# Kernel tuning notes

Hardware: AMD Instinct MI355X
Metric: run time of the kernel (lower is better)

The kernel has to match this reference:

```python
import jax, jax.numpy as jnp
import numpy as np

HEADS = 8
DIM_HEAD = 64


def setup_inputs() -> dict:
    key = jax.random.key(0)
    k1, k2, k3 = jax.random.split(key, 3)
    B, C, L = 8, 512, 8192
    hidden = HEADS * DIM_HEAD  # 512
    x = jax.random.normal(k1, (B, C, L), dtype=jnp.float32)
    W_qkv = jax.random.normal(k2, (3 * hidden, C), dtype=jnp.float32) * (1.0 / np.sqrt(C))
    W_out = jax.random.normal(k3, (C, hidden), dtype=jnp.float32) * (1.0 / np.sqrt(hidden))
    b_out = jnp.zeros((C,), dtype=jnp.float32)
    return {"x": x, "W_qkv": W_qkv, "W_out": W_out, "b_out": b_out}


def reference(x, W_qkv, W_out, b_out):
    b, c, l = x.shape
    h, d = HEADS, DIM_HEAD
    # pointwise conv1d == channel matmul: [3*h*d, c] x [b, c, l] -> [b, 3*h*d, l]
    qkv = jnp.einsum('oc,bcl->bol', W_qkv, x)
    q, k, v = jnp.split(qkv, 3, axis=1)
    q = q.reshape(b, h, d, l)
    k = jax.nn.softmax(k.reshape(b, h, d, l), axis=-1)
    v = v.reshape(b, h, d, l)
    # context = k @ v^T : [b,h,d,d]
    context = jnp.einsum('bhdl,bhel->bhde', k, v)
    # out = context^T @ q : [b,h,e,l]
    out = jnp.einsum('bhde,bhdl->bhel', context, q)
    out = out.reshape(b, h * d, l)
    # to_out pointwise conv with bias
    return jnp.einsum('ch,bhl->bcl', W_out, out) + b_out[None, :, None]
```

## Files before the change

### kernel.cpp

```cpp
#include <hip/hip_runtime.h>
#include <hip/hip_bf16.h>

typedef unsigned short u16;
typedef __attribute__((ext_vector_type(8))) short s16x8;
typedef __attribute__((ext_vector_type(4))) float f32x4;

__device__ __forceinline__ u16 f2bf(float f) {
  union { float f; unsigned u; } v; v.f = f;
  unsigned r = (v.u + 0x7fffu + ((v.u >> 16) & 1u)) >> 16;
  return (u16)r;
}
__device__ __forceinline__ float bf2f(u16 u) {
  union { unsigned u; float f; } v; v.u = ((unsigned)u) << 16;
  return v.f;
}
__device__ __forceinline__ void gld_lds16(const void* g, void* l) {
  __builtin_amdgcn_global_load_lds(
      (const __attribute__((address_space(1))) void*)g,
      (__attribute__((address_space(3))) void*)l, 16, 0, 0);
}
__device__ __forceinline__ s16x8 dsr128(const u16* p) {
  s16x8 r;
  asm volatile("ds_read_b128 %0, %1"
               : "=v"(r)
               : "v"((const __attribute__((address_space(3))) u16*)p));
  return r;
}

__global__ void prep_w(const float* __restrict__ Wqkv, const float* __restrict__ Woutf,
                       u16* __restrict__ Wkv2, u16* __restrict__ WqT, u16* __restrict__ Wout) {
  int i = blockIdx.x * 256 + threadIdx.x;
  {
    int o = i >> 9, c = i & 511;
    int h = o >> 7, r = o & 127;
    int src = (r < 64) ? (512 + h * 64 + r) : (1024 + h * 64 + (r - 64));
    Wkv2[i] = f2bf(Wqkv[src * 512 + c]);
  }
  if (i < 262144) {
    int c = i >> 9, o = i & 511;
    WqT[i]  = f2bf(Wqkv[o * 512 + c]);
    Wout[i] = f2bf(Woutf[i]);
  }
}

__global__ __launch_bounds__(256) void prep_x(const float* __restrict__ x, u16* __restrict__ xt) {
  __shared__ float t[32][33];
  int l0 = blockIdx.x * 32, c0 = blockIdx.y * 32;
  size_t b = blockIdx.z;
  int tid = threadIdx.x;
  int r = tid >> 3, q = tid & 7;
  const float4 v = *(const float4*)(x + (b * 512 + c0 + r) * 8192 + l0 + q * 4);
  t[r][q * 4 + 0] = v.x; t[r][q * 4 + 1] = v.y;
  t[r][q * 4 + 2] = v.z; t[r][q * 4 + 3] = v.w;
  __syncthreads();
  ushort4 o;
  o.x = f2bf(t[q * 4 + 0][r]); o.y = f2bf(t[q * 4 + 1][r]);
  o.z = f2bf(t[q * 4 + 2][r]); o.w = f2bf(t[q * 4 + 3][r]);
  *(ushort4*)(xt + (b * 8192 + l0 + r) * 512 + c0 + q * 4) = o;
}

__global__ __launch_bounds__(256) void gemm_bt(
    const u16* __restrict__ A, size_t sA,
    const u16* __restrict__ BT, size_t sB,
    u16* __restrict__ Cv, size_t sC,
    int N, int K)
{
  __shared__ u16 lsa[128 * 32];
  __shared__ u16 lsb[128 * 32];
  int tid = threadIdx.x, wid = tid >> 6, lane = tid & 63;
  int m0 = blockIdx.y << 7, n0 = blockIdx.x << 7;
  const u16* Ab = A + (size_t)blockIdx.z * sA;
  const u16* Bb = BT + (size_t)blockIdx.z * sB;
  int fr = lane & 15, kg = lane >> 4;
  int wr = wid >> 1, wc = wid & 1;
  int f0 = tid, f1 = tid + 256;
  const u16* pA0 = Ab + (size_t)(m0 + (f0 >> 2)) * K + (f0 & 3) * 8;
  const u16* pA1 = Ab + (size_t)(m0 + (f1 >> 2)) * K + (f1 & 3) * 8;
  const u16* pB0 = Bb + (size_t)(n0 + (f0 >> 2)) * K + (f0 & 3) * 8;
  const u16* pB1 = Bb + (size_t)(n0 + (f1 >> 2)) * K + (f1 & 3) * 8;
  u16* dA0 = &lsa[wid * 512];
  u16* dA1 = &lsa[(wid + 4) * 512];
  u16* dB0 = &lsb[wid * 512];
  u16* dB1 = &lsb[(wid + 4) * 512];
  f32x4 acc[4][4] = {};
  for (int kt = 0; kt < K; kt += 32) {
    gld_lds16(pA0, dA0); gld_lds16(pA1, dA1);
    gld_lds16(pB0, dB0); gld_lds16(pB1, dB1);
    pA0 += 32; pA1 += 32; pB0 += 32; pB1 += 32;
    __syncthreads();
    s16x8 af[4], bf_[4];
#pragma unroll
    for (int mi = 0; mi < 4; ++mi)
      af[mi] = *(const s16x8*)&lsa[(wr * 64 + mi * 16 + fr) * 32 + kg * 8];
#pragma unroll
    for (int ni = 0; ni < 4; ++ni)
      bf_[ni] = *(const s16x8*)&lsb[(wc * 64 + ni * 16 + fr) * 32 + kg * 8];
#pragma unroll
    for (int mi = 0; mi < 4; ++mi)
#pragma unroll
      for (int ni = 0; ni < 4; ++ni)
        acc[mi][ni] = __builtin_amdgcn_mfma_f32_16x16x32_bf16(af[mi], bf_[ni], acc[mi][ni], 0, 0, 0);
    __syncthreads();
  }
  int r0 = m0 + wr * 64 + kg * 4;
  int c0 = n0 + wc * 64 + fr;
  u16* C = Cv + (size_t)blockIdx.z * sC;
#pragma unroll
  for (int mi = 0; mi < 4; ++mi)
#pragma unroll
    for (int ni = 0; ni < 4; ++ni)
#pragma unroll
      for (int j = 0; j < 4; ++j)
        C[(size_t)(r0 + mi * 16 + j) * N + (c0 + ni * 16)] = f2bf(acc[mi][ni][j]);
}

__global__ __launch_bounds__(256, 4) void gemm_ctx(
    const u16* __restrict__ A,
    const u16* __restrict__ BT, size_t sB,
    float* __restrict__ E, float* __restrict__ Z)
{
  __shared__ u16 pool[17408];
  const int tid = threadIdx.x, wid = tid >> 6, lane = tid & 63;
  const int fr = lane & 15, kg = lane >> 4;
  const int wr = wid >> 1, wc = wid & 1;

  const int nwg = (int)gridDim.x;
  const int bx = (int)blockIdx.x;
  const int id = (bx & 7) * (nwg >> 3) + (bx >> 3);
  const int my = id % 8;
  const int t2 = id / 8;
  const int nx = t2 % 64;
  const int z  = t2 / 64;
  const int m0 = my << 7, n0 = nx << 7;
  const u16* Ab = A + (size_t)m0 * 512;
  const u16* Bb = BT + (size_t)z * sB + (size_t)n0 * 512;

  const int P0 = tid, P1 = tid + 256;
  int b2_, s_, t_;
  b2_ = P0 >> 3; s_ = P0 & 7; t_ = (s_ - b2_) & 7;
  const size_t g0 = (size_t)((b2_ << 1) + (t_ >> 2)) * 512 + (t_ & 3) * 8;
  b2_ = P1 >> 3; s_ = P1 & 7; t_ = (s_ - b2_) & 7;
  const size_t g1 = (size_t)((b2_ << 1) + (t_ >> 2)) * 512 + (t_ & 3) * 8;

  int aoff[4], boff[4];
#pragma unroll
  for (int i = 0; i < 4; ++i) {
    int ra = wr * 64 + i * 16 + fr;
    aoff[i] = (ra >> 1) * 64 + ((((ra & 1) << 2) + kg + (ra >> 1)) & 7) * 8;
    int rb = wc * 64 + i * 16 + fr;
    boff[i] = (rb >> 1) * 64 + ((((rb & 1) << 2) + kg + (rb >> 1)) & 7) * 8;
  }

  auto stage = [&](int sl, int kt) {
    gld_lds16(Ab + g0 + kt, &pool[sl * 4096 + P0 * 8]);
    gld_lds16(Ab + g1 + kt, &pool[sl * 4096 + P1 * 8]);
    gld_lds16(Bb + g0 + kt, &pool[8192 + sl * 4096 + P0 * 8]);
    gld_lds16(Bb + g1 + kt, &pool[8192 + sl * 4096 + P1 * 8]);
  };

  f32x4 acc[4][4] = {};
  stage(0, 0);
#pragma unroll
  for (int k = 0; k < 16; ++k) {
    if (k < 15) stage((k + 1) & 1, (k + 1) * 32);
    if (k < 15) { asm volatile("s_waitcnt vmcnt(4)" ::: "memory"); }
    else        { asm volatile("s_waitcnt vmcnt(0)" ::: "memory"); }
    __builtin_amdgcn_s_barrier();
    s16x8 af[4], bf_[4];
    const u16* la = &pool[(k & 1) * 4096];
    const u16* lb = &pool[8192 + (k & 1) * 4096];
#pragma unroll
    for (int mi = 0; mi < 4; ++mi) af[mi] = dsr128(la + aoff[mi]);
#pragma unroll
    for (int ni = 0; ni < 4; ++ni) bf_[ni] = dsr128(lb + boff[ni]);
    asm volatile("s_waitcnt lgkmcnt(0)" ::: "memory");
    __builtin_amdgcn_sched_barrier(0);
    __builtin_amdgcn_s_setprio(1);
#pragma unroll
    for (int mi = 0; mi < 4; ++mi)
#pragma unroll
      for (int ni = 0; ni < 4; ++ni)
        acc[mi][ni] = __builtin_amdgcn_mfma_f32_16x16x32_bf16(af[mi], bf_[ni], acc[mi][ni], 0, 0, 0);
    __builtin_amdgcn_s_setprio(0);
    __builtin_amdgcn_s_barrier();
  }

  const size_t bh = (size_t)z * 8 + my;
  u16* kbuf = pool;
  u16* vbuf = pool + 64 * 136;
#pragma unroll
  for (int mi = 0; mi < 4; ++mi)
#pragma unroll
    for (int ni = 0; ni < 4; ++ni)
#pragma unroll
      for (int j = 0; j < 4; ++j) {
        int r = mi * 16 + kg * 4 + j;
        int l = wc * 64 + ni * 16 + fr;
        float vv = acc[mi][ni][j];
        if (wr == 0) kbuf[r * 136 + l] = f2bf(__expf(vv));
        else         vbuf[r * 136 + l] = f2bf(vv);
      }
  __syncthreads();
  {
    int d = tid >> 2, q = tid & 3;
    float s = 0.f;
#pragma unroll
    for (int i = 0; i < 4; ++i) {
      s16x8 k8 = *(const s16x8*)&kbuf[d * 136 + q * 32 + i * 8];
#pragma unroll
      for (int j = 0; j < 8; ++j) s += bf2f((u16)k8[j]);
    }
    s += __shfl_xor(s, 1);
    s += __shfl_xor(s, 2);
    if (q == 0) atomicAdd(&Z[bh * 64 + d], s);
  }
  f32x4 eacc[4] = {};
#pragma unroll
  for (int ks = 0; ks < 4; ++ks) {
    s16x8 ka = *(const s16x8*)&kbuf[(wid * 16 + fr) * 136 + ks * 32 + kg * 8];
#pragma unroll
    for (int n2 = 0; n2 < 4; ++n2) {
      s16x8 vb = *(const s16x8*)&vbuf[(n2 * 16 + fr) * 136 + ks * 32 + kg * 8];
      eacc[n2] = __builtin_amdgcn_mfma_f32_16x16x32_bf16(ka, vb, eacc[n2], 0, 0, 0);
    }
  }
  float* Eb = E + bh * 4096;
#pragma unroll
  for (int n2 = 0; n2 < 4; ++n2)
#pragma unroll
    for (int j = 0; j < 4; ++j)
      atomicAdd(&Eb[(wid * 16 + kg * 4 + j) * 64 + n2 * 16 + fr], eacc[n2][j]);
}

__global__ __launch_bounds__(256, 4) void gemm128f(
    const u16* __restrict__ A, size_t sA,
    const u16* __restrict__ BT, size_t sB,
    float* __restrict__ Cv, size_t sC,
    const float* __restrict__ bias,
    int Mt, int Nt)
{
  __shared__ u16 lsa[2][4096];
  __shared__ u16 lsb[2][4096];
  const int tid = threadIdx.x, wid = tid >> 6, lane = tid & 63;
  const int fr = lane & 15, kg = lane >> 4;
  const int wr = wid >> 1, wc = wid & 1;

  const int nwg = (int)gridDim.x;
  const int bx = (int)blockIdx.x;
  const int id = (bx & 7) * (nwg >> 3) + (bx >> 3);
  const int my = id % Mt;
  const int t2 = id / Mt;
  const int nx = t2 % Nt;
  const int z  = t2 / Nt;
  const int m0 = my << 7, n0 = nx << 7;
  const u16* Ab = A + (size_t)z * sA;
  const u16* Bb = BT + (size_t)z * sB;

  const int P0 = tid, P1 = tid + 256;
  int b2_, s_, t_;
  b2_ = P0 >> 3; s_ = P0 & 7; t_ = (s_ - b2_) & 7;
  const size_t g0 = (size_t)((b2_ << 1) + (t_ >> 2)) * 512 + (t_ & 3) * 8;
  b2_ = P1 >> 3; s_ = P1 & 7; t_ = (s_ - b2_) & 7;
  const size_t g1 = (size_t)((b2_ << 1) + (t_ >> 2)) * 512 + (t_ & 3) * 8;
  const u16* paG0 = Ab + (size_t)m0 * 512 + g0;
  const u16* paG1 = Ab + (size_t)m0 * 512 + g1;
  const u16* pbG0 = Bb + (size_t)n0 * 512 + g0;
  const u16* pbG1 = Bb + (size_t)n0 * 512 + g1;

  int aoff[4], boff[4];
#pragma unroll
  for (int i = 0; i < 4; ++i) {
    int ra = wr * 64 + i * 16 + fr;
    aoff[i] = (ra >> 1) * 64 + ((((ra & 1) << 2) + kg + (ra >> 1)) & 7) * 8;
    int rb = wc * 64 + i * 16 + fr;
    boff[i] = (rb >> 1) * 64 + ((((rb & 1) << 2) + kg + (rb >> 1)) & 7) * 8;
  }

  auto stage = [&](int sl, int kt) {
    gld_lds16(paG0 + kt, &lsa[sl][P0 * 8]);
    gld_lds16(paG1 + kt, &lsa[sl][P1 * 8]);
    gld_lds16(pbG0 + kt, &lsb[sl][P0 * 8]);
    gld_lds16(pbG1 + kt, &lsb[sl][P1 * 8]);
  };

  f32x4 acc[4][4] = {};
  stage(0, 0);
#pragma unroll
  for (int k = 0; k < 16; ++k) {
    if (k < 15) stage((k + 1) & 1, (k + 1) * 32);
    if (k < 15) { asm volatile("s_waitcnt vmcnt(4)" ::: "memory"); }
    else        { asm volatile("s_waitcnt vmcnt(0)" ::: "memory"); }
    __builtin_amdgcn_s_barrier();
    s16x8 af[4], bf_[4];
    const u16* la = lsa[k & 1];
    const u16* lb = lsb[k & 1];
#pragma unroll
    for (int mi = 0; mi < 4; ++mi) af[mi] = dsr128(la + aoff[mi]);
#pragma unroll
    for (int ni = 0; ni < 4; ++ni) bf_[ni] = dsr128(lb + boff[ni]);
    asm volatile("s_waitcnt lgkmcnt(0)" ::: "memory");
    __builtin_amdgcn_sched_barrier(0);
    __builtin_amdgcn_s_setprio(1);
#pragma unroll
    for (int mi = 0; mi < 4; ++mi)
#pragma unroll
      for (int ni = 0; ni < 4; ++ni)
        acc[mi][ni] = __builtin_amdgcn_mfma_f32_16x16x32_bf16(af[mi], bf_[ni], acc[mi][ni], 0, 0, 0);
    __builtin_amdgcn_s_setprio(0);
    __builtin_amdgcn_s_barrier();
  }

  const int r0 = m0 + wr * 64 + kg * 4;
  const int c0 = n0 + wc * 64 + fr;
  float* C = Cv + (size_t)z * sC;
#pragma unroll
  for (int mi = 0; mi < 4; ++mi)
#pragma unroll
    for (int j = 0; j < 4; ++j) {
      float bv = bias[r0 + mi * 16 + j];
#pragma unroll
      for (int ni = 0; ni < 4; ++ni)
        C[(size_t)(r0 + mi * 16 + j) * 8192 + (c0 + ni * 16)] = acc[mi][ni][j] + bv;
    }
}

__global__ __launch_bounds__(256) void m1_fused(const float* __restrict__ E, const float* __restrict__ Z,
                                                const u16* __restrict__ Wout, u16* __restrict__ M1) {
  int cb = blockIdx.x, h = blockIdx.y, b = blockIdx.z;
  __shared__ float ctx[64][65];
  __shared__ float zs[64];
  int tid = threadIdx.x;
  size_t bh = (size_t)(b * 8 + h);
  const float* Eb = E + bh * 4096;
  if (tid < 64) zs[tid] = Z[bh * 64 + tid];
  __syncthreads();
  for (int i = tid; i < 4096; i += 256)
    ctx[i >> 6][i & 63] = Eb[i] / zs[i >> 6];
  __syncthreads();
  int d = tid & 63;
  int hbase = h * 64;
  for (int ci = 0; ci < 16; ++ci) {
    int c = __builtin_amdgcn_readfirstlane(cb * 64 + (tid >> 6) + ci * 4);
    const u16* wrow = Wout + c * 512 + hbase;
    float a0 = 0.f, a1 = 0.f, a2 = 0.f, a3 = 0.f;
#pragma unroll
    for (int e = 0; e < 64; e += 4) {
      a0 += bf2f(wrow[e + 0]) * ctx[d][e + 0];
      a1 += bf2f(wrow[e + 1]) * ctx[d][e + 1];
      a2 += bf2f(wrow[e + 2]) * ctx[d][e + 2];
      a3 += bf2f(wrow[e + 3]) * ctx[d][e + 3];
    }
    M1[((size_t)b * 512 + c) * 512 + hbase + d] = f2bf((a0 + a1) + (a2 + a3));
  }
}

extern "C" void kernel_launch(void* const* d_in, const int* in_sizes, int n_in,
                              void* d_out, int out_size, void* d_ws, size_t ws_size,
                              hipStream_t stream) {
  const float* x     = (const float*)d_in[0];
  const float* Wqkv  = (const float*)d_in[1];
  const float* Woutf = (const float*)d_in[2];
  const float* bout  = (const float*)d_in[3];
  char* ws = (char*)d_ws;
  u16*  xt  = (u16*)ws;
  u16*  Wkv2= (u16*)(ws + 201326592);
  u16*  WqT = (u16*)(ws + 202375168);
  u16*  Wo  = (u16*)(ws + 202899456);
  u16*  M1  = (u16*)(ws + 203423744);
  u16*  G   = (u16*)(ws + 207618048);
  float* E  = (float*)(ws + 211812352);
  float* Z  = (float*)(ws + 212860928);

  hipMemsetAsync(ws + 211812352, 0, 1048576 + 16384, stream);
  prep_w<<<2048, 256, 0, stream>>>(Wqkv, Woutf, Wkv2, WqT, Wo);
  prep_x<<<dim3(256, 16, 8), 256, 0, stream>>>(x, xt);
  gemm_ctx<<<4096, 256, 0, stream>>>(Wkv2, xt, (size_t)8192 * 512, E, Z);
  m1_fused<<<dim3(8, 8, 8), 256, 0, stream>>>(E, Z, Wo, M1);
  gemm_bt<<<dim3(4, 4, 8), 256, 0, stream>>>(M1, (size_t)512 * 512, WqT, 0,
                                             G, (size_t)512 * 512, 512, 512);
  gemm128f<<<2048, 256, 0, stream>>>(G, (size_t)512 * 512, xt, (size_t)8192 * 512,
                                     (float*)d_out, (size_t)512 * 8192, bout, 4, 64);
}
```

Before: 231.3 us.

## Enlarge gemm_ctx tile to 256 rows with 512-thread blocks sharing x loads

The context GEMM block now covers two heads (256 rows of K/V weights) with 8 waves instead of 128 rows with 4 waves. Each x tile loaded into LDS is reused across twice as many output rows, which halves redundant global reads of the large activation tensor and halves the grid size. In exchange the block needs twice the LDS and more threads per block, which may lower occupancy. The epilogue is extended to do the softmax sums and k·vᵀ context for two heads per block.

```diff
diff --git a/kernel.cpp b/kernel.cpp
--- a/kernel.cpp
+++ b/kernel.cpp
@@ -114,48 +114,46 @@
         C[(size_t)(r0 + mi * 16 + j) * N + (c0 + ni * 16)] = f2bf(acc[mi][ni][j]);
 }
 
-__global__ __launch_bounds__(256, 4) void gemm_ctx(
+__global__ __launch_bounds__(512, 4) void gemm_ctx(
     const u16* __restrict__ A,
     const u16* __restrict__ BT, size_t sB,
     float* __restrict__ E, float* __restrict__ Z)
 {
-  __shared__ u16 pool[17408];
+  __shared__ u16 pool[34816];
   const int tid = threadIdx.x, wid = tid >> 6, lane = tid & 63;
   const int fr = lane & 15, kg = lane >> 4;
-  const int wr = wid >> 1, wc = wid & 1;
+  const int wm = wid >> 1, wc = wid & 1;
 
   const int nwg = (int)gridDim.x;
   const int bx = (int)blockIdx.x;
   const int id = (bx & 7) * (nwg >> 3) + (bx >> 3);
-  const int my = id % 8;
-  const int t2 = id / 8;
+  const int my = id % 4;
+  const int t2 = id / 4;
   const int nx = t2 % 64;
   const int z  = t2 / 64;
-  const int m0 = my << 7, n0 = nx << 7;
+  const int m0 = my << 8, n0 = nx << 7;
   const u16* Ab = A + (size_t)m0 * 512;
   const u16* Bb = BT + (size_t)z * sB + (size_t)n0 * 512;
 
-  const int P0 = tid, P1 = tid + 256;
-  int b2_, s_, t_;
-  b2_ = P0 >> 3; s_ = P0 & 7; t_ = (s_ - b2_) & 7;
-  const size_t g0 = (size_t)((b2_ << 1) + (t_ >> 2)) * 512 + (t_ & 3) * 8;
-  b2_ = P1 >> 3; s_ = P1 & 7; t_ = (s_ - b2_) & 7;
-  const size_t g1 = (size_t)((b2_ << 1) + (t_ >> 2)) * 512 + (t_ & 3) * 8;
+  auto gsw = [](int P) -> size_t {
+    int b2 = P >> 3, s = P & 7, t = (s - b2) & 7;
+    return (size_t)((b2 << 1) + (t >> 2)) * 512 + (t & 3) * 8;
+  };
+  const size_t gA0 = gsw(tid), gA1 = gsw(tid + 512), gB0 = gsw(tid);
 
   int aoff[4], boff[4];
 #pragma unroll
   for (int i = 0; i < 4; ++i) {
-    int ra = wr * 64 + i * 16 + fr;
+    int ra = wm * 64 + i * 16 + fr;
     aoff[i] = (ra >> 1) * 64 + ((((ra & 1) << 2) + kg + (ra >> 1)) & 7) * 8;
     int rb = wc * 64 + i * 16 + fr;
     boff[i] = (rb >> 1) * 64 + ((((rb & 1) << 2) + kg + (rb >> 1)) & 7) * 8;
   }
 
   auto stage = [&](int sl, int kt) {
-    gld_lds16(Ab + g0 + kt, &pool[sl * 4096 + P0 * 8]);
-    gld_lds16(Ab + g1 + kt, &pool[sl * 4096 + P1 * 8]);
-    gld_lds16(Bb + g0 + kt, &pool[8192 + sl * 4096 + P0 * 8]);
-    gld_lds16(Bb + g1 + kt, &pool[8192 + sl * 4096 + P1 * 8]);
+    gld_lds16(Ab + gA0 + kt, &pool[sl * 8192 + tid * 8]);
+    gld_lds16(Ab + gA1 + kt, &pool[sl * 8192 + 4096 + tid * 8]);
+    gld_lds16(Bb + gB0 + kt, &pool[16384 + sl * 4096 + tid * 8]);
   };
 
   f32x4 acc[4][4] = {};
@@ -163,12 +161,12 @@
 #pragma unroll
   for (int k = 0; k < 16; ++k) {
     if (k < 15) stage((k + 1) & 1, (k + 1) * 32);
-    if (k < 15) { asm volatile("s_waitcnt vmcnt(4)" ::: "memory"); }
+    if (k < 15) { asm volatile("s_waitcnt vmcnt(3)" ::: "memory"); }
     else        { asm volatile("s_waitcnt vmcnt(0)" ::: "memory"); }
     __builtin_amdgcn_s_barrier();
     s16x8 af[4], bf_[4];
-    const u16* la = &pool[(k & 1) * 4096];
-    const u16* lb = &pool[8192 + (k & 1) * 4096];
+    const u16* la = &pool[(k & 1) * 8192];
+    const u16* lb = &pool[16384 + (k & 1) * 4096];
 #pragma unroll
     for (int mi = 0; mi < 4; ++mi) af[mi] = dsr128(la + aoff[mi]);
 #pragma unroll
@@ -185,51 +183,59 @@
     __builtin_amdgcn_s_barrier();
   }
 
-  const size_t bh = (size_t)z * 8 + my;
-  u16* kbuf = pool;
-  u16* vbuf = pool + 64 * 136;
-#pragma unroll
-  for (int mi = 0; mi < 4; ++mi)
-#pragma unroll
-    for (int ni = 0; ni < 4; ++ni)
-#pragma unroll
-      for (int j = 0; j < 4; ++j) {
-        int r = mi * 16 + kg * 4 + j;
-        int l = wc * 64 + ni * 16 + fr;
-        float vv = acc[mi][ni][j];
-        if (wr == 0) kbuf[r * 136 + l] = f2bf(__expf(vv));
-        else         vbuf[r * 136 + l] = f2bf(vv);
-      }
+  {
+    const int h = wm >> 1, isV = wm & 1;
+    u16* kb = pool + h * 17408;
+    u16* vb = kb + 8704;
+#pragma unroll
+    for (int mi = 0; mi < 4; ++mi)
+#pragma unroll
+      for (int ni = 0; ni < 4; ++ni)
+#pragma unroll
+        for (int j = 0; j < 4; ++j) {
+          int r = mi * 16 + kg * 4 + j;
+          int l = wc * 64 + ni * 16 + fr;
+          float vv = acc[mi][ni][j];
+          if (!isV) kb[r * 136 + l] = f2bf(__expf(vv));
+          else      vb[r * 136 + l] = f2bf(vv);
+        }
+  }
   __syncthreads();
   {
-    int d = tid >> 2, q = tid & 3;
+    int h2 = tid >> 8, d = (tid >> 2) & 63, q = tid & 3;
+    const u16* kb = pool + h2 * 17408;
     float s = 0.f;
 #pragma unroll
     for (int i = 0; i < 4; ++i) {
-      s16x8 k8 = *(const s16x8*)&kbuf[d * 136 + q * 32 + i * 8];
+      s16x8 k8 = *(const s16x8*)&kb[d * 136 + q * 32 + i * 8];
 #pragma unroll
       for (int j = 0; j < 8; ++j) s += bf2f((u16)k8[j]);
     }
     s += __shfl_xor(s, 1);
     s += __shfl_xor(s, 2);
-    if (q == 0) atomicAdd(&Z[bh * 64 + d], s);
-  }
-  f32x4 eacc[4] = {};
-#pragma unroll
-  for (int ks = 0; ks < 4; ++ks) {
-    s16x8 ka = *(const s16x8*)&kbuf[(wid * 16 + fr) * 136 + ks * 32 + kg * 8];
-#pragma unroll
-    for (int n2 = 0; n2 < 4; ++n2) {
-      s16x8 vb = *(const s16x8*)&vbuf[(n2 * 16 + fr) * 136 + ks * 32 + kg * 8];
-      eacc[n2] = __builtin_amdgcn_mfma_f32_16x16x32_bf16(ka, vb, eacc[n2], 0, 0, 0);
+    if (q == 0) atomicAdd(&Z[((size_t)z * 8 + my * 2 + h2) * 64 + d], s);
+  }
+  {
+    const int eh = wid >> 2, strip = wid & 3;
+    const u16* kb = pool + eh * 17408;
+    const u16* vb = kb + 8704;
+    f32x4 eacc[4] = {};
+#pragma unroll
+    for (int ks = 0; ks < 4; ++ks) {
+      s16x8 ka = *(const s16x8*)&kb[(strip * 16 + fr) * 136 + ks * 32 + kg * 8];
+#pragma unroll
+      for (int n2 = 0; n2 < 4; ++n2) {
+        s16x8 vbf = *(const s16x8*)&vb[(n2 * 16 + fr) * 136 + ks * 32 + kg * 8];
+        eacc[n2] = __builtin_amdgcn_mfma_f32_16x16x32_bf16(ka, vbf, eacc[n2], 0, 0, 0);
+      }
     }
-  }
-  float* Eb = E + bh * 4096;
-#pragma unroll
-  for (int n2 = 0; n2 < 4; ++n2)
-#pragma unroll
-    for (int j = 0; j < 4; ++j)
-      atomicAdd(&Eb[(wid * 16 + kg * 4 + j) * 64 + n2 * 16 + fr], eacc[n2][j]);
+    float* Eb = E + ((size_t)z * 8 + my * 2 + eh) * 4096;
+#pragma unroll
+    for (int n2 = 0; n2 < 4; ++n2)
+#pragma unroll
+      for (int j = 0; j < 4; ++j)
+        atomicAdd(&Eb[(strip * 16 + kg * 4 + j) * 64 + n2 * 16 + fr], eacc[n2][j]);
+  }
 }
 
 __global__ __launch_bounds__(256, 4) void gemm128f(
@@ -374,7 +380,7 @@
   hipMemsetAsync(ws + 211812352, 0, 1048576 + 16384, stream);
   prep_w<<<2048, 256, 0, stream>>>(Wqkv, Woutf, Wkv2, WqT, Wo);
   prep_x<<<dim3(256, 16, 8), 256, 0, stream>>>(x, xt);
-  gemm_ctx<<<4096, 256, 0, stream>>>(Wkv2, xt, (size_t)8192 * 512, E, Z);
+  gemm_ctx<<<2048, 512, 0, stream>>>(Wkv2, xt, (size_t)8192 * 512, E, Z);
   m1_fused<<<dim3(8, 8, 8), 256, 0, stream>>>(E, Z, Wo, M1);
   gemm_bt<<<dim3(4, 4, 8), 256, 0, stream>>>(M1, (size_t)512 * 512, WqT, 0,
                                              G, (size_t)512 * 512, 512, 512);
```

After: 244.2 us. +5.6%, slower.
